# Performance work log

Hardware: AMD Instinct MI355X
Metric: run time of the kernel (lower is better)

The kernel has to match this reference:

```python
import jax, jax.numpy as jnp
import numpy as np

B, QL, KVL, DQ, DKV = 8192, 24, 24, 12, 512


def setup_inputs() -> dict:
    key = jax.random.key(0)
    ks = jax.random.split(key, 9)
    s = lambda fan_in: 1.0 / np.sqrt(fan_in)
    return {
        "q": jax.random.normal(ks[0], (B, QL, DQ), jnp.float32),
        "k": jax.random.normal(ks[1], (B, KVL, DKV), jnp.float32),
        "v": jax.random.normal(ks[2], (B, KVL, DKV), jnp.float32),
        "Wq": jax.random.uniform(ks[3], (DQ, DQ), jnp.float32, -s(DQ), s(DQ)),
        "bq": jax.random.uniform(ks[4], (DQ,), jnp.float32, -s(DQ), s(DQ)),
        "Wk": jax.random.uniform(ks[5], (DQ, DKV), jnp.float32, -s(DKV), s(DKV)),
        "bk": jax.random.uniform(ks[6], (DQ,), jnp.float32, -s(DKV), s(DKV)),
        "Wl": jax.random.uniform(ks[7], (DQ, KVL), jnp.float32, -s(KVL), s(KVL)),
        "bl": jax.random.uniform(ks[8], (DQ,), jnp.float32, -s(KVL), s(KVL)),
    }


def reference(q, k, v, Wq, bq, Wk, bk, Wl, bl):
    # q: [b, q_len, dim_q], k: [b, kv_len, dim_kv]; v is unused (as in source).
    q_proj = jnp.einsum("bqd,ed->bqe", q, Wq) + bq          # [b, q_len, dim_q]
    k_proj = jnp.einsum("bkf,ef->bke", k, Wk) + bk          # [b, kv_len, dim_q]
    qk = jnp.einsum("bqe,bke->bqk", q_proj, k_proj)          # [b, q_len, kv_len]
    a_q = jax.nn.softmax(qk, axis=1)                         # softmax over q_len
    a_k = jax.nn.softmax(qk, axis=2)                         # softmax over kv_len
    c_q = jnp.einsum("bqk,bke->bqe", a_q, k_proj)            # [b, q_len, dim_q]
    qc = jnp.concatenate([q, c_q], axis=2)                   # [b, q_len, 2*dim_q]
    c_k = jnp.einsum("bqk,bqe->bke", a_k, qc)                # [b, kv_len, 2*dim_q]
    # linear over kv_len (== seq_len) dim: c_k^T [b, 2*dim_q, kv_len] -> [b, 2*dim_q, dim_q]
    attn = jnp.einsum("bke,dk->bed", c_k, Wl) + bl
    return attn
```

## Files before the change

### kernel.cpp

```cpp
#include <hip/hip_runtime.h>


typedef short s16x8 __attribute__((ext_vector_type(8)));
typedef float f32x4 __attribute__((ext_vector_type(4)));

__device__ __forceinline__ unsigned perm_hi(float a, float b) {
  return __builtin_amdgcn_perm(__float_as_uint(a), __float_as_uint(b), 0x07060302u);
}

#define DPP_ADD(x, ctrl, rmask)                                                   \
  x += __int_as_float(__builtin_amdgcn_update_dpp(                                \
      0, __float_as_int(x), ctrl, rmask, 0xF, false))

__device__ __forceinline__ float wave_sum64(float x) {
  DPP_ADD(x, 0xB1, 0xF);
  DPP_ADD(x, 0x4E, 0xF);
  DPP_ADD(x, 0x141, 0xF);
  DPP_ADD(x, 0x140, 0xF);
  DPP_ADD(x, 0x142, 0xA);
  DPP_ADD(x, 0x143, 0xC);
  return x;
}

#define DPP_BF(x, OP, ctrl)                                                       \
  {                                                                               \
    float _t = __int_as_float(__builtin_amdgcn_update_dpp(                        \
        0, __float_as_int(x), ctrl, 0xF, 0xF, true));                             \
    x = OP(x, _t);                                                                \
  }
__device__ __forceinline__ float bf32_max(float x) {
  DPP_BF(x, fmaxf, 0xB1);
  DPP_BF(x, fmaxf, 0x4E);
  DPP_BF(x, fmaxf, 0x141);
  DPP_BF(x, fmaxf, 0x140);
  float t = __int_as_float(__builtin_amdgcn_ds_swizzle(__float_as_int(x), 0x401F));
  return fmaxf(x, t);
}
__device__ __forceinline__ float bf32_add(float x) {
  DPP_ADD(x, 0xB1, 0xF);
  DPP_ADD(x, 0x4E, 0xF);
  DPP_ADD(x, 0x141, 0xF);
  DPP_ADD(x, 0x140, 0xF);
  float t = __int_as_float(__builtin_amdgcn_ds_swizzle(__float_as_int(x), 0x401F));
  return x + t;
}

__device__ __forceinline__ float dot12(const float* a, float4 b0, float4 b1, float4 b2) {
  return a[0] * b0.x + a[1] * b0.y + a[2] * b0.z + a[3] * b0.w +
         a[4] * b1.x + a[5] * b1.y + a[6] * b1.z + a[7] * b1.w +
         a[8] * b2.x + a[9] * b2.y + a[10] * b2.z + a[11] * b2.w;
}

__global__ __launch_bounds__(384, 3) void coattn_fused(
    const float* __restrict__ q, const float* __restrict__ k,
    const float* __restrict__ Wq, const float* __restrict__ bq,
    const float* __restrict__ Wk, const float* __restrict__ bk,
    const float* __restrict__ Wl, const float* __restrict__ bl,
    float* __restrict__ out) {
  constexpr int WPAD = 520;

  __shared__ alignas(16) char smemA[12 * WPAD * 2 * 2];
  __shared__ alignas(16) float kpL[96][12];

  short* lwk_hi = (short*)smemA;
  short* lwk_lo = (short*)(smemA + 12 * WPAD * 2);

  const int tid = threadIdx.x;
  const int wave = tid >> 6;
  const int lane = tid & 63;

  for (int i = tid; i < 12 * 512; i += 384) {
    const int e = i >> 9, d = i & 511;
    const float f = Wk[i];
    const unsigned u = __float_as_uint(f);
    const float lo = f - __uint_as_float(u & 0xFFFF0000u);
    lwk_hi[e * WPAD + d] = (short)(u >> 16);
    lwk_lo[e * WPAD + d] = (short)(__float_as_uint(lo) >> 16);
  }
  __syncthreads();

  const int rowL = lane & 15;
  const int kgrp = lane >> 4;
  const int e_eff = (rowL < 12) ? rowL : 11;

  const int r0 = blockIdx.x * 96 + wave * 16;
  const float* abase = k + (size_t)(r0 + rowL) * 512 + kgrp * 8;
  const short* bhi_base = &lwk_hi[e_eff * WPAD + kgrp * 8];
  const short* blo_base = &lwk_lo[e_eff * WPAD + kgrp * 8];

  f32x4 acc = {0.f, 0.f, 0.f, 0.f};

#define COMP(X0, X1, S)                                                            \
  {                                                                                \
    s16x8 bhi = *(const s16x8*)(bhi_base + (S)*32);                                \
    s16x8 blo = *(const s16x8*)(blo_base + (S)*32);                                \
    union { unsigned u[4]; s16x8 v; } ah, al;                                      \
    ah.u[0] = perm_hi((X0).y, (X0).x);                                             \
    ah.u[1] = perm_hi((X0).w, (X0).z);                                             \
    ah.u[2] = perm_hi((X1).y, (X1).x);                                             \
    ah.u[3] = perm_hi((X1).w, (X1).z);                                             \
    float l0 = (X0).x - __uint_as_float(__float_as_uint((X0).x) & 0xFFFF0000u);    \
    float l1 = (X0).y - __uint_as_float(__float_as_uint((X0).y) & 0xFFFF0000u);    \
    float l2 = (X0).z - __uint_as_float(__float_as_uint((X0).z) & 0xFFFF0000u);    \
    float l3 = (X0).w - __uint_as_float(__float_as_uint((X0).w) & 0xFFFF0000u);    \
    float l4 = (X1).x - __uint_as_float(__float_as_uint((X1).x) & 0xFFFF0000u);    \
    float l5 = (X1).y - __uint_as_float(__float_as_uint((X1).y) & 0xFFFF0000u);    \
    float l6 = (X1).z - __uint_as_float(__float_as_uint((X1).z) & 0xFFFF0000u);    \
    float l7 = (X1).w - __uint_as_float(__float_as_uint((X1).w) & 0xFFFF0000u);    \
    al.u[0] = perm_hi(l1, l0);                                                     \
    al.u[1] = perm_hi(l3, l2);                                                     \
    al.u[2] = perm_hi(l5, l4);                                                     \
    al.u[3] = perm_hi(l7, l6);                                                     \
    acc = __builtin_amdgcn_mfma_f32_16x16x32_bf16(ah.v, bhi, acc, 0, 0, 0);        \
    acc = __builtin_amdgcn_mfma_f32_16x16x32_bf16(ah.v, blo, acc, 0, 0, 0);        \
    acc = __builtin_amdgcn_mfma_f32_16x16x32_bf16(al.v, bhi, acc, 0, 0, 0);        \
  }

#define LOADS(SA, SB, R)                                                           \
  SA = *(const float4*)(abase + (R)*32);                                           \
  SB = *(const float4*)(abase + (R)*32 + 4);

  {
    float4 A0a, A0b, A1a, A1b, A2a, A2b, A3a, A3b;
    float4 A4a, A4b, A5a, A5b, A6a, A6b, A7a, A7b;
    LOADS(A0a, A0b, 0)
    LOADS(A1a, A1b, 1)
    LOADS(A2a, A2b, 2)
    LOADS(A3a, A3b, 3)
    LOADS(A4a, A4b, 4)
    LOADS(A5a, A5b, 5)
    LOADS(A6a, A6b, 6)   COMP(A0a, A0b, 0)
    LOADS(A7a, A7b, 7)   COMP(A1a, A1b, 1)
    LOADS(A0a, A0b, 8)   COMP(A2a, A2b, 2)
    LOADS(A1a, A1b, 9)   COMP(A3a, A3b, 3)
    LOADS(A2a, A2b, 10)  COMP(A4a, A4b, 4)
    LOADS(A3a, A3b, 11)  COMP(A5a, A5b, 5)
    LOADS(A4a, A4b, 12)  COMP(A6a, A6b, 6)
    LOADS(A5a, A5b, 13)  COMP(A7a, A7b, 7)
    LOADS(A6a, A6b, 14)  COMP(A0a, A0b, 8)
    LOADS(A7a, A7b, 15)  COMP(A1a, A1b, 9)
    COMP(A2a, A2b, 10)
    COMP(A3a, A3b, 11)
    COMP(A4a, A4b, 12)
    COMP(A5a, A5b, 13)
    COMP(A6a, A6b, 14)
    COMP(A7a, A7b, 15)
  }
#undef LOADS
#undef COMP

  if (rowL < 12) {
    const int lr0 = wave * 16 + kgrp * 4;
#pragma unroll
    for (int i = 0; i < 4; ++i) kpL[lr0 + i][rowL] = acc[i];
  }
  __syncthreads();

  if (wave < 4) {
    float(*qcS)[28] = (float(*)[28])(smemA + (size_t)wave * (24 * 28 * 4));
    float(*GS)[12] = (float(*)[12])(smemA + 4 * (24 * 28 * 4) + (size_t)wave * (24 * 12 * 4));

    const int b = blockIdx.x * 4 + wave;
    const int li = (lane < 24) ? lane : 0;
    const bool act = (lane < 24);
    const int kb0 = wave * 24;

    const float4* WqV = reinterpret_cast<const float4*>(Wq);
    const float4* WlV = reinterpret_cast<const float4*>(Wl);

    float qr[12];
    if (act) {
      const float4* qb = reinterpret_cast<const float4*>(q + (size_t)b * 288 + li * 12);
      float4 t0 = qb[0], t1 = qb[1], t2 = qb[2];
      qr[0] = t0.x; qr[1] = t0.y; qr[2] = t0.z; qr[3] = t0.w;
      qr[4] = t1.x; qr[5] = t1.y; qr[6] = t1.z; qr[7] = t1.w;
      qr[8] = t2.x; qr[9] = t2.y; qr[10] = t2.z; qr[11] = t2.w;
    } else {
#pragma unroll
      for (int d = 0; d < 12; ++d) qr[d] = 0.f;
    }

    float qp_[12];
#pragma unroll
    for (int e = 0; e < 12; ++e) {
      float4 w0 = WqV[e * 3 + 0], w1 = WqV[e * 3 + 1], w2 = WqV[e * 3 + 2];
      qp_[e] = bq[e] + dot12(qr, w0, w1, w2);
    }

    float qbk = 0.f;
#pragma unroll
    for (int e = 0; e < 12; ++e) qbk += qp_[e] * bk[e];

    float qkr[24];
#pragma unroll
    for (int kk = 0; kk < 24; ++kk) {
      float4 k0 = *(const float4*)&kpL[kb0 + kk][0];
      float4 k1 = *(const float4*)&kpL[kb0 + kk][4];
      float4 k2 = *(const float4*)&kpL[kb0 + kk][8];
      qkr[kk] = qbk + dot12(qp_, k0, k1, k2);
    }
    if (lane >= 24) {
#pragma unroll
      for (int j = 0; j < 24; ++j) qkr[j] = -1e30f;
    }

    float akr[24];
    {
      float rm = qkr[0];
#pragma unroll
      for (int j = 1; j < 24; ++j) rm = fmaxf(rm, qkr[j]);
      float s = 0.f;
#pragma unroll
      for (int j = 0; j < 24; ++j) {
        akr[j] = __expf(qkr[j] - rm);
        s += akr[j];
      }
      const float inv = __builtin_amdgcn_rcpf(s);
#pragma unroll
      for (int j = 0; j < 24; ++j) akr[j] *= inv;
    }

    if (lane < 32) {
#pragma unroll
      for (int j = 0; j < 24; ++j) {
        const float m = bf32_max(qkr[j]);
        const float t = __expf(qkr[j] - m);
        const float s2 = bf32_add(t);
        qkr[j] = t * __builtin_amdgcn_rcpf(s2);
      }
    }

    float sa = 0.f;
#pragma unroll
    for (int j = 0; j < 24; ++j) sa += qkr[j];
    float cq[12];
#pragma unroll
    for (int e = 0; e < 12; ++e) cq[e] = bk[e] * sa;
#pragma unroll
    for (int kk = 0; kk < 24; ++kk) {
      float4 k0 = *(const float4*)&kpL[kb0 + kk][0];
      float4 k1 = *(const float4*)&kpL[kb0 + kk][4];
      float4 k2 = *(const float4*)&kpL[kb0 + kk][8];
      const float a = qkr[kk];
      cq[0] += a * k0.x; cq[1] += a * k0.y; cq[2] += a * k0.z; cq[3] += a * k0.w;
      cq[4] += a * k1.x; cq[5] += a * k1.y; cq[6] += a * k1.z; cq[7] += a * k1.w;
      cq[8] += a * k2.x; cq[9] += a * k2.y; cq[10] += a * k2.z; cq[11] += a * k2.w;
    }

    float G[12];
#pragma unroll
    for (int d = 0; d < 12; ++d) {
      float4 w0 = WlV[d * 6 + 0], w1 = WlV[d * 6 + 1], w2 = WlV[d * 6 + 2];
      float4 w3 = WlV[d * 6 + 3], w4 = WlV[d * 6 + 4], w5 = WlV[d * 6 + 5];
      G[d] = akr[0] * w0.x + akr[1] * w0.y + akr[2] * w0.z + akr[3] * w0.w +
             akr[4] * w1.x + akr[5] * w1.y + akr[6] * w1.z + akr[7] * w1.w +
             akr[8] * w2.x + akr[9] * w2.y + akr[10] * w2.z + akr[11] * w2.w +
             akr[12] * w3.x + akr[13] * w3.y + akr[14] * w3.z + akr[15] * w3.w +
             akr[16] * w4.x + akr[17] * w4.y + akr[18] * w4.z + akr[19] * w4.w +
             akr[20] * w5.x + akr[21] * w5.y + akr[22] * w5.z + akr[23] * w5.w;
    }

    if (act) {
      float4 t;
      t.x = qr[0]; t.y = qr[1]; t.z = qr[2]; t.w = qr[3];
      *(float4*)&qcS[li][0] = t;
      t.x = qr[4]; t.y = qr[5]; t.z = qr[6]; t.w = qr[7];
      *(float4*)&qcS[li][4] = t;
      t.x = qr[8]; t.y = qr[9]; t.z = qr[10]; t.w = qr[11];
      *(float4*)&qcS[li][8] = t;
      t.x = cq[0]; t.y = cq[1]; t.z = cq[2]; t.w = cq[3];
      *(float4*)&qcS[li][12] = t;
      t.x = cq[4]; t.y = cq[5]; t.z = cq[6]; t.w = cq[7];
      *(float4*)&qcS[li][16] = t;
      t.x = cq[8]; t.y = cq[9]; t.z = cq[10]; t.w = cq[11];
      *(float4*)&qcS[li][20] = t;
      t.x = G[0]; t.y = G[1]; t.z = G[2]; t.w = G[3];
      *(float4*)&GS[li][0] = t;
      t.x = G[4]; t.y = G[5]; t.z = G[6]; t.w = G[7];
      *(float4*)&GS[li][4] = t;
      t.x = G[8]; t.y = G[9]; t.z = G[10]; t.w = G[11];
      *(float4*)&GS[li][8] = t;
    }

    if (act) {
      float accq[12];
#pragma unroll
      for (int d = 0; d < 12; ++d) accq[d] = bl[d];
#pragma unroll
      for (int q0 = 0; q0 < 24; ++q0) {
        const float qv = qcS[q0][li];
        float4 g0 = *(const float4*)&GS[q0][0];
        float4 g1 = *(const float4*)&GS[q0][4];
        float4 g2 = *(const float4*)&GS[q0][8];
        accq[0] += qv * g0.x; accq[1] += qv * g0.y; accq[2] += qv * g0.z; accq[3] += qv * g0.w;
        accq[4] += qv * g1.x; accq[5] += qv * g1.y; accq[6] += qv * g1.z; accq[7] += qv * g1.w;
        accq[8] += qv * g2.x; accq[9] += qv * g2.y; accq[10] += qv * g2.z; accq[11] += qv * g2.w;
      }
      float* ob = out + (size_t)b * 288 + li * 12;
      float4 w0, w1, w2;
      w0.x = accq[0]; w0.y = accq[1]; w0.z = accq[2]; w0.w = accq[3];
      w1.x = accq[4]; w1.y = accq[5]; w1.z = accq[6]; w1.w = accq[7];
      w2.x = accq[8]; w2.y = accq[9]; w2.z = accq[10]; w2.w = accq[11];
      *(float4*)(ob + 0) = w0;
      *(float4*)(ob + 4) = w1;
      *(float4*)(ob + 8) = w2;
    }
  }
}

__global__ __launch_bounds__(64) void coattn_kernel(
    const float* __restrict__ q, const float* __restrict__ k,
    const float* __restrict__ Wq, const float* __restrict__ bq,
    const float* __restrict__ Wk, const float* __restrict__ bk,
    const float* __restrict__ Wl, const float* __restrict__ bl,
    float* __restrict__ out) {
  constexpr int QL = 24, KVL = 24, DQ = 12, DKV = 512;

  __shared__ alignas(16) float kp[KVL][DQ];
  __shared__ alignas(16) float qc[QL][24];
  __shared__ alignas(16) float akT[KVL][28];
  __shared__ alignas(16) float ckL[KVL][28];
  __shared__ alignas(16) float WqL[DQ][DQ];
  __shared__ alignas(16) float WlT[KVL][DQ];
  __shared__ alignas(16) float bqL[DQ], bkL[DQ], blL[DQ];

  const int lane = threadIdx.x;
  const int b = blockIdx.x;
  const int li = (lane < 24) ? lane : 0;

  for (int p = lane; p < DQ * DQ; p += 64) WqL[p / DQ][p % DQ] = Wq[p];
  for (int p = lane; p < DQ * KVL; p += 64) WlT[p % KVL][p / KVL] = Wl[p];
  const float* qb = q + (size_t)b * (QL * DQ);
  for (int p = lane; p < QL * DQ; p += 64) qc[p / DQ][p % DQ] = qb[p];
  if (lane < DQ) {
    bqL[lane] = bq[lane];
    bkL[lane] = bk[lane];
    blL[lane] = bl[lane];
  }

  const float4* WkV = reinterpret_cast<const float4*>(Wk);
  float4 wk0[DQ], wk1[DQ];
#pragma unroll
  for (int e = 0; e < DQ; ++e) {
    wk0[e] = WkV[e * 128 + lane];
    wk1[e] = WkV[e * 128 + 64 + lane];
  }

  const float4* kbV = reinterpret_cast<const float4*>(k + (size_t)b * (KVL * DKV));

#define KROW(AC, BC, ROW)                                                          \
  {                                                                                \
    float pp[DQ];                                                                  \
    _Pragma("unroll") for (int e = 0; e < DQ; ++e) {                               \
      pp[e] = (AC).x * wk0[e].x + (AC).y * wk0[e].y + (AC).z * wk0[e].z +          \
              (AC).w * wk0[e].w + (BC).x * wk1[e].x + (BC).y * wk1[e].y +          \
              (BC).z * wk1[e].z + (BC).w * wk1[e].w;                               \
    }                                                                              \
    _Pragma("unroll") for (int e = 0; e < DQ; ++e) pp[e] = wave_sum64(pp[e]);      \
    if (lane == 63) {                                                              \
      float4 w0, w1, w2;                                                           \
      w0.x = pp[0]; w0.y = pp[1]; w0.z = pp[2]; w0.w = pp[3];                      \
      w1.x = pp[4]; w1.y = pp[5]; w1.z = pp[6]; w1.w = pp[7];                      \
      w2.x = pp[8]; w2.y = pp[9]; w2.z = pp[10]; w2.w = pp[11];                    \
      *(float4*)&kp[ROW][0] = w0;                                                  \
      *(float4*)&kp[ROW][4] = w1;                                                  \
      *(float4*)&kp[ROW][8] = w2;                                                  \
    }                                                                              \
  }

  float4 A0 = kbV[0 * 128 + lane], B0 = kbV[0 * 128 + 64 + lane];
  float4 A1 = kbV[1 * 128 + lane], B1 = kbV[1 * 128 + 64 + lane];
  float4 A2, B2, A3, B3;
  for (int kv = 0; kv < KVL; kv += 4) {
    {
      const int r = kv + 2;
      A2 = kbV[r * 128 + lane];
      B2 = kbV[r * 128 + 64 + lane];
    }
    KROW(A0, B0, kv);
    {
      const int r = kv + 3;
      A3 = kbV[r * 128 + lane];
      B3 = kbV[r * 128 + 64 + lane];
    }
    KROW(A1, B1, kv + 1);
    {
      const int r = (kv + 4 < KVL) ? kv + 4 : KVL - 1;
      A0 = kbV[r * 128 + lane];
      B0 = kbV[r * 128 + 64 + lane];
    }
    KROW(A2, B2, kv + 2);
    {
      const int r = (kv + 5 < KVL) ? kv + 5 : KVL - 1;
      A1 = kbV[r * 128 + lane];
      B1 = kbV[r * 128 + 64 + lane];
    }
    KROW(A3, B3, kv + 3);
  }
#undef KROW

  float qr[DQ];
  {
    float4 t0 = *(const float4*)&qc[li][0];
    float4 t1 = *(const float4*)&qc[li][4];
    float4 t2 = *(const float4*)&qc[li][8];
    qr[0] = t0.x; qr[1] = t0.y; qr[2] = t0.z; qr[3] = t0.w;
    qr[4] = t1.x; qr[5] = t1.y; qr[6] = t1.z; qr[7] = t1.w;
    qr[8] = t2.x; qr[9] = t2.y; qr[10] = t2.z; qr[11] = t2.w;
  }
  float bqr[DQ];
  {
    float4 t0 = *(const float4*)&bqL[0];
    float4 t1 = *(const float4*)&bqL[4];
    float4 t2 = *(const float4*)&bqL[8];
    bqr[0] = t0.x; bqr[1] = t0.y; bqr[2] = t0.z; bqr[3] = t0.w;
    bqr[4] = t1.x; bqr[5] = t1.y; bqr[6] = t1.z; bqr[7] = t1.w;
    bqr[8] = t2.x; bqr[9] = t2.y; bqr[10] = t2.z; bqr[11] = t2.w;
  }
  float qp_[DQ];
#pragma unroll
  for (int e = 0; e < DQ; ++e) {
    float4 w0 = *(const float4*)&WqL[e][0];
    float4 w1 = *(const float4*)&WqL[e][4];
    float4 w2 = *(const float4*)&WqL[e][8];
    qp_[e] = bqr[e] + dot12(qr, w0, w1, w2);
  }

  float bkr[DQ];
  {
    float4 t0 = *(const float4*)&bkL[0];
    float4 t1 = *(const float4*)&bkL[4];
    float4 t2 = *(const float4*)&bkL[8];
    bkr[0] = t0.x; bkr[1] = t0.y; bkr[2] = t0.z; bkr[3] = t0.w;
    bkr[4] = t1.x; bkr[5] = t1.y; bkr[6] = t1.z; bkr[7] = t1.w;
    bkr[8] = t2.x; bkr[9] = t2.y; bkr[10] = t2.z; bkr[11] = t2.w;
  }
  float qbk = 0.f;
#pragma unroll
  for (int e = 0; e < DQ; ++e) qbk += qp_[e] * bkr[e];

  float qkr[KVL];
#pragma unroll
  for (int kk = 0; kk < KVL; ++kk) {
    float4 k0 = *(const float4*)&kp[kk][0];
    float4 k1 = *(const float4*)&kp[kk][4];
    float4 k2 = *(const float4*)&kp[kk][8];
    qkr[kk] = qbk + dot12(qp_, k0, k1, k2);
  }
  if (lane >= 24 && lane < 32) {
#pragma unroll
    for (int j = 0; j < KVL; ++j) qkr[j] = -1e30f;
  }

  float akr[KVL];
  {
    float rm = qkr[0];
#pragma unroll
    for (int j = 1; j < KVL; ++j) rm = fmaxf(rm, qkr[j]);
    float s = 0.f;
#pragma unroll
    for (int j = 0; j < KVL; ++j) {
      akr[j] = __expf(qkr[j] - rm);
      s += akr[j];
    }
    const float inv = __builtin_amdgcn_rcpf(s);
#pragma unroll
    for (int j = 0; j < KVL; ++j) akr[j] *= inv;
  }

#pragma unroll
  for (int j = 0; j < KVL; ++j) {
    const float m = bf32_max(qkr[j]);
    const float t = __expf(qkr[j] - m);
    const float s2 = bf32_add(t);
    qkr[j] = t * __builtin_amdgcn_rcpf(s2);
  }

  float sa = 0.f;
#pragma unroll
  for (int j = 0; j < KVL; ++j) sa += qkr[j];
  float cq[DQ];
#pragma unroll
  for (int e = 0; e < DQ; ++e) cq[e] = bkr[e] * sa;
#pragma unroll
  for (int kk = 0; kk < KVL; ++kk) {
    float4 k0 = *(const float4*)&kp[kk][0];
    float4 k1 = *(const float4*)&kp[kk][4];
    float4 k2 = *(const float4*)&kp[kk][8];
    const float a = qkr[kk];
    cq[0] += a * k0.x; cq[1] += a * k0.y; cq[2] += a * k0.z; cq[3] += a * k0.w;
    cq[4] += a * k1.x; cq[5] += a * k1.y; cq[6] += a * k1.z; cq[7] += a * k1.w;
    cq[8] += a * k2.x; cq[9] += a * k2.y; cq[10] += a * k2.z; cq[11] += a * k2.w;
  }
  if (lane < 24) {
    float4 w0, w1, w2;
    w0.x = cq[0]; w0.y = cq[1]; w0.z = cq[2]; w0.w = cq[3];
    w1.x = cq[4]; w1.y = cq[5]; w1.z = cq[6]; w1.w = cq[7];
    w2.x = cq[8]; w2.y = cq[9]; w2.z = cq[10]; w2.w = cq[11];
    *(float4*)&qc[li][12] = w0;
    *(float4*)&qc[li][16] = w1;
    *(float4*)&qc[li][20] = w2;
#pragma unroll
    for (int kk = 0; kk < KVL; ++kk) akT[kk][li] = akr[kk];
  }

  float ak[QL];
  {
    float4 a0 = *(const float4*)&akT[li][0];
    float4 a1 = *(const float4*)&akT[li][4];
    float4 a2 = *(const float4*)&akT[li][8];
    float4 a3 = *(const float4*)&akT[li][12];
    float4 a4 = *(const float4*)&akT[li][16];
    float4 a5 = *(const float4*)&akT[li][20];
    ak[0] = a0.x; ak[1] = a0.y; ak[2] = a0.z; ak[3] = a0.w;
    ak[4] = a1.x; ak[5] = a1.y; ak[6] = a1.z; ak[7] = a1.w;
    ak[8] = a2.x; ak[9] = a2.y; ak[10] = a2.z; ak[11] = a2.w;
    ak[12] = a3.x; ak[13] = a3.y; ak[14] = a3.z; ak[15] = a3.w;
    ak[16] = a4.x; ak[17] = a4.y; ak[18] = a4.z; ak[19] = a4.w;
    ak[20] = a5.x; ak[21] = a5.y; ak[22] = a5.z; ak[23] = a5.w;
  }
  float ck[24];
#pragma unroll
  for (int e = 0; e < 24; ++e) ck[e] = 0.f;
#pragma unroll
  for (int qq = 0; qq < QL; ++qq) {
    float4 c0 = *(const float4*)&qc[qq][0];
    float4 c1 = *(const float4*)&qc[qq][4];
    float4 c2 = *(const float4*)&qc[qq][8];
    float4 c3 = *(const float4*)&qc[qq][12];
    float4 c4 = *(const float4*)&qc[qq][16];
    float4 c5 = *(const float4*)&qc[qq][20];
    const float a = ak[qq];
    ck[0] += a * c0.x; ck[1] += a * c0.y; ck[2] += a * c0.z; ck[3] += a * c0.w;
    ck[4] += a * c1.x; ck[5] += a * c1.y; ck[6] += a * c1.z; ck[7] += a * c1.w;
    ck[8] += a * c2.x; ck[9] += a * c2.y; ck[10] += a * c2.z; ck[11] += a * c2.w;
    ck[12] += a * c3.x; ck[13] += a * c3.y; ck[14] += a * c3.z; ck[15] += a * c3.w;
    ck[16] += a * c4.x; ck[17] += a * c4.y; ck[18] += a * c4.z; ck[19] += a * c4.w;
    ck[20] += a * c5.x; ck[21] += a * c5.y; ck[22] += a * c5.z; ck[23] += a * c5.w;
  }
  if (lane < 24) {
    float4 w0, w1, w2, w3, w4, w5;
    w0.x = ck[0]; w0.y = ck[1]; w0.z = ck[2]; w0.w = ck[3];
    w1.x = ck[4]; w1.y = ck[5]; w1.z = ck[6]; w1.w = ck[7];
    w2.x = ck[8]; w2.y = ck[9]; w2.z = ck[10]; w2.w = ck[11];
    w3.x = ck[12]; w3.y = ck[13]; w3.z = ck[14]; w3.w = ck[15];
    w4.x = ck[16]; w4.y = ck[17]; w4.z = ck[18]; w4.w = ck[19];
    w5.x = ck[20]; w5.y = ck[21]; w5.z = ck[22]; w5.w = ck[23];
    *(float4*)&ckL[li][0] = w0;
    *(float4*)&ckL[li][4] = w1;
    *(float4*)&ckL[li][8] = w2;
    *(float4*)&ckL[li][12] = w3;
    *(float4*)&ckL[li][16] = w4;
    *(float4*)&ckL[li][20] = w5;
  }

  float acc[DQ];
  {
    float4 t0 = *(const float4*)&blL[0];
    float4 t1 = *(const float4*)&blL[4];
    float4 t2 = *(const float4*)&blL[8];
    acc[0] = t0.x; acc[1] = t0.y; acc[2] = t0.z; acc[3] = t0.w;
    acc[4] = t1.x; acc[5] = t1.y; acc[6] = t1.z; acc[7] = t1.w;
    acc[8] = t2.x; acc[9] = t2.y; acc[10] = t2.z; acc[11] = t2.w;
  }
#pragma unroll
  for (int kk = 0; kk < KVL; ++kk) {
    const float cv = ckL[kk][li];
    float4 w0 = *(const float4*)&WlT[kk][0];
    float4 w1 = *(const float4*)&WlT[kk][4];
    float4 w2 = *(const float4*)&WlT[kk][8];
    acc[0] += cv * w0.x; acc[1] += cv * w0.y; acc[2] += cv * w0.z; acc[3] += cv * w0.w;
    acc[4] += cv * w1.x; acc[5] += cv * w1.y; acc[6] += cv * w1.z; acc[7] += cv * w1.w;
    acc[8] += cv * w2.x; acc[9] += cv * w2.y; acc[10] += cv * w2.z; acc[11] += cv * w2.w;
  }
  if (lane < 24) {
    float* ob = out + (size_t)b * 288 + li * 12;
    float4 w0, w1, w2;
    w0.x = acc[0]; w0.y = acc[1]; w0.z = acc[2]; w0.w = acc[3];
    w1.x = acc[4]; w1.y = acc[5]; w1.z = acc[6]; w1.w = acc[7];
    w2.x = acc[8]; w2.y = acc[9]; w2.z = acc[10]; w2.w = acc[11];
    *(float4*)(ob + 0) = w0;
    *(float4*)(ob + 4) = w1;
    *(float4*)(ob + 8) = w2;
  }
}

extern "C" void kernel_launch(void* const* d_in, const int* in_sizes, int n_in,
                              void* d_out, int out_size, void* d_ws, size_t ws_size,
                              hipStream_t stream) {
  const float* q = (const float*)d_in[0];
  const float* k = (const float*)d_in[1];
  const float* Wq = (const float*)d_in[3];
  const float* bq = (const float*)d_in[4];
  const float* Wk = (const float*)d_in[5];
  const float* bk = (const float*)d_in[6];
  const float* Wl = (const float*)d_in[7];
  const float* bl = (const float*)d_in[8];
  float* out = (float*)d_out;

  const int B = in_sizes[0] / (24 * 12);

  if ((B % 4) == 0) {
    coattn_fused<<<B / 4, 384, 0, stream>>>(q, k, Wq, bq, Wk, bk, Wl, bl, out);
  } else {
    coattn_kernel<<<B, 64, 0, stream>>>(q, k, Wq, bq, Wk, bk, Wl, bl, out);
  }
}
```

Before: 115.3 us.

## Stage k rows through double-buffered per-wave LDS for coalesced global loads

Global reads of k now follow a row-contiguous pattern: each group of 16 lanes reads 256 contiguous bytes of one row, and the data is written into a per-wave, double-buffered LDS tile. The MFMA operands are then read back from LDS in the layout the bf16 split-precision multiply needs. The aim is better global memory coalescing and load/compute overlap on the bandwidth-bound k projection. In exchange it adds about 52KB of LDS, which likely limits residency to fewer blocks per CU, and it reuses the Wk staging area for kpL.

```diff
diff --git a/kernel.cpp b/kernel.cpp
--- a/kernel.cpp
+++ b/kernel.cpp
@@ -57,13 +57,14 @@
     const float* __restrict__ Wk, const float* __restrict__ bk,
     const float* __restrict__ Wl, const float* __restrict__ bl,
     float* __restrict__ out) {
-  constexpr int WPAD = 520;
-
-  __shared__ alignas(16) char smemA[12 * WPAD * 2 * 2];
-  __shared__ alignas(16) float kpL[96][12];
-
-  short* lwk_hi = (short*)smemA;
-  short* lwk_lo = (short*)(smemA + 12 * WPAD * 2);
+  constexpr int WPADS = 520;
+  constexpr int KSTRF = 68;
+
+  __shared__ alignas(16) char smemW[12 * WPADS * 2 * 2];
+  __shared__ alignas(16) char smemK[6 * 2 * 16 * KSTRF * 4];
+
+  short* lwk_hi = (short*)smemW;
+  short* lwk_lo = (short*)(smemW + 12 * WPADS * 2);
 
   const int tid = threadIdx.x;
   const int wave = tid >> 6;
@@ -74,39 +75,55 @@
     const float f = Wk[i];
     const unsigned u = __float_as_uint(f);
     const float lo = f - __uint_as_float(u & 0xFFFF0000u);
-    lwk_hi[e * WPAD + d] = (short)(u >> 16);
-    lwk_lo[e * WPAD + d] = (short)(__float_as_uint(lo) >> 16);
+    lwk_hi[e * WPADS + d] = (short)(u >> 16);
+    lwk_lo[e * WPADS + d] = (short)(__float_as_uint(lo) >> 16);
   }
   __syncthreads();
 
   const int rowL = lane & 15;
   const int kgrp = lane >> 4;
   const int e_eff = (rowL < 12) ? rowL : 11;
+  const int sub = lane >> 4;
+  const int pos = lane & 15;
 
   const int r0 = blockIdx.x * 96 + wave * 16;
-  const float* abase = k + (size_t)(r0 + rowL) * 512 + kgrp * 8;
-  const short* bhi_base = &lwk_hi[e_eff * WPAD + kgrp * 8];
-  const short* blo_base = &lwk_lo[e_eff * WPAD + kgrp * 8];
+  const float* kg = k + (size_t)(r0 + sub) * 512 + pos * 4;
+  float* kw = (float*)smemK + wave * (2 * 16 * KSTRF);
 
   f32x4 acc = {0.f, 0.f, 0.f, 0.f};
 
-#define COMP(X0, X1, S)                                                            \
+#define LOADU(R, C)                                                                \
+  R##0 = *(const float4*)(kg + 0 * 2048 + (C)*64);                                 \
+  R##1 = *(const float4*)(kg + 1 * 2048 + (C)*64);                                 \
+  R##2 = *(const float4*)(kg + 2 * 2048 + (C)*64);                                 \
+  R##3 = *(const float4*)(kg + 3 * 2048 + (C)*64);
+
+#define WRITEU(R, BUF)                                                             \
+  *(float4*)&kw[(BUF)*16 * KSTRF + (0 * 4 + sub) * KSTRF + pos * 4] = R##0;        \
+  *(float4*)&kw[(BUF)*16 * KSTRF + (1 * 4 + sub) * KSTRF + pos * 4] = R##1;        \
+  *(float4*)&kw[(BUF)*16 * KSTRF + (2 * 4 + sub) * KSTRF + pos * 4] = R##2;        \
+  *(float4*)&kw[(BUF)*16 * KSTRF + (3 * 4 + sub) * KSTRF + pos * 4] = R##3;
+
+#define STEP(C, S)                                                                 \
   {                                                                                \
-    s16x8 bhi = *(const s16x8*)(bhi_base + (S)*32);                                \
-    s16x8 blo = *(const s16x8*)(blo_base + (S)*32);                                \
+    const float* kb = &kw[((C)&1) * 16 * KSTRF];                                   \
+    float4 f0 = *(const float4*)&kb[rowL * KSTRF + kgrp * 8 + (S)*32];             \
+    float4 f1 = *(const float4*)&kb[rowL * KSTRF + kgrp * 8 + (S)*32 + 4];         \
+    s16x8 bhi = *(const s16x8*)(lwk_hi + e_eff * WPADS + kgrp * 8 + (2 * (C) + (S)) * 32); \
+    s16x8 blo = *(const s16x8*)(lwk_lo + e_eff * WPADS + kgrp * 8 + (2 * (C) + (S)) * 32); \
     union { unsigned u[4]; s16x8 v; } ah, al;                                      \
-    ah.u[0] = perm_hi((X0).y, (X0).x);                                             \
-    ah.u[1] = perm_hi((X0).w, (X0).z);                                             \
-    ah.u[2] = perm_hi((X1).y, (X1).x);                                             \
-    ah.u[3] = perm_hi((X1).w, (X1).z);                                             \
-    float l0 = (X0).x - __uint_as_float(__float_as_uint((X0).x) & 0xFFFF0000u);    \
-    float l1 = (X0).y - __uint_as_float(__float_as_uint((X0).y) & 0xFFFF0000u);    \
-    float l2 = (X0).z - __uint_as_float(__float_as_uint((X0).z) & 0xFFFF0000u);    \
-    float l3 = (X0).w - __uint_as_float(__float_as_uint((X0).w) & 0xFFFF0000u);    \
-    float l4 = (X1).x - __uint_as_float(__float_as_uint((X1).x) & 0xFFFF0000u);    \
-    float l5 = (X1).y - __uint_as_float(__float_as_uint((X1).y) & 0xFFFF0000u);    \
-    float l6 = (X1).z - __uint_as_float(__float_as_uint((X1).z) & 0xFFFF0000u);    \
-    float l7 = (X1).w - __uint_as_float(__float_as_uint((X1).w) & 0xFFFF0000u);    \
+    ah.u[0] = perm_hi(f0.y, f0.x);                                                 \
+    ah.u[1] = perm_hi(f0.w, f0.z);                                                 \
+    ah.u[2] = perm_hi(f1.y, f1.x);                                                 \
+    ah.u[3] = perm_hi(f1.w, f1.z);                                                 \
+    float l0 = f0.x - __uint_as_float(__float_as_uint(f0.x) & 0xFFFF0000u);        \
+    float l1 = f0.y - __uint_as_float(__float_as_uint(f0.y) & 0xFFFF0000u);        \
+    float l2 = f0.z - __uint_as_float(__float_as_uint(f0.z) & 0xFFFF0000u);        \
+    float l3 = f0.w - __uint_as_float(__float_as_uint(f0.w) & 0xFFFF0000u);        \
+    float l4 = f1.x - __uint_as_float(__float_as_uint(f1.x) & 0xFFFF0000u);        \
+    float l5 = f1.y - __uint_as_float(__float_as_uint(f1.y) & 0xFFFF0000u);        \
+    float l6 = f1.z - __uint_as_float(__float_as_uint(f1.z) & 0xFFFF0000u);        \
+    float l7 = f1.w - __uint_as_float(__float_as_uint(f1.w) & 0xFFFF0000u);        \
     al.u[0] = perm_hi(l1, l0);                                                     \
     al.u[1] = perm_hi(l3, l2);                                                     \
     al.u[2] = perm_hi(l5, l4);                                                     \
@@ -116,39 +133,29 @@
     acc = __builtin_amdgcn_mfma_f32_16x16x32_bf16(al.v, bhi, acc, 0, 0, 0);        \
   }
 
-#define LOADS(SA, SB, R)                                                           \
-  SA = *(const float4*)(abase + (R)*32);                                           \
-  SB = *(const float4*)(abase + (R)*32 + 4);
+#define COMPUTE(C) STEP(C, 0) STEP(C, 1)
 
   {
-    float4 A0a, A0b, A1a, A1b, A2a, A2b, A3a, A3b;
-    float4 A4a, A4b, A5a, A5b, A6a, A6b, A7a, A7b;
-    LOADS(A0a, A0b, 0)
-    LOADS(A1a, A1b, 1)
-    LOADS(A2a, A2b, 2)
-    LOADS(A3a, A3b, 3)
-    LOADS(A4a, A4b, 4)
-    LOADS(A5a, A5b, 5)
-    LOADS(A6a, A6b, 6)   COMP(A0a, A0b, 0)
-    LOADS(A7a, A7b, 7)   COMP(A1a, A1b, 1)
-    LOADS(A0a, A0b, 8)   COMP(A2a, A2b, 2)
-    LOADS(A1a, A1b, 9)   COMP(A3a, A3b, 3)
-    LOADS(A2a, A2b, 10)  COMP(A4a, A4b, 4)
-    LOADS(A3a, A3b, 11)  COMP(A5a, A5b, 5)
-    LOADS(A4a, A4b, 12)  COMP(A6a, A6b, 6)
-    LOADS(A5a, A5b, 13)  COMP(A7a, A7b, 7)
-    LOADS(A6a, A6b, 14)  COMP(A0a, A0b, 8)
-    LOADS(A7a, A7b, 15)  COMP(A1a, A1b, 9)
-    COMP(A2a, A2b, 10)
-    COMP(A3a, A3b, 11)
-    COMP(A4a, A4b, 12)
-    COMP(A5a, A5b, 13)
-    COMP(A6a, A6b, 14)
-    COMP(A7a, A7b, 15)
-  }
-#undef LOADS
-#undef COMP
-
+    float4 X0, X1, X2, X3, Y0, Y1, Y2, Y3;
+    LOADU(X, 0)
+    LOADU(Y, 1)
+    WRITEU(X, 0)
+    LOADU(X, 2)  WRITEU(Y, 1)  COMPUTE(0)
+    LOADU(Y, 3)  WRITEU(X, 0)  COMPUTE(1)
+    LOADU(X, 4)  WRITEU(Y, 1)  COMPUTE(2)
+    LOADU(Y, 5)  WRITEU(X, 0)  COMPUTE(3)
+    LOADU(X, 6)  WRITEU(Y, 1)  COMPUTE(4)
+    LOADU(Y, 7)  WRITEU(X, 0)  COMPUTE(5)
+    WRITEU(Y, 1)  COMPUTE(6)
+    COMPUTE(7)
+  }
+#undef LOADU
+#undef WRITEU
+#undef STEP
+#undef COMPUTE
+
+  __syncthreads();
+  float(*kpL)[12] = (float(*)[12])smemW;
   if (rowL < 12) {
     const int lr0 = wave * 16 + kgrp * 4;
 #pragma unroll
@@ -157,8 +164,8 @@
   __syncthreads();
 
   if (wave < 4) {
-    float(*qcS)[28] = (float(*)[28])(smemA + (size_t)wave * (24 * 28 * 4));
-    float(*GS)[12] = (float(*)[12])(smemA + 4 * (24 * 28 * 4) + (size_t)wave * (24 * 12 * 4));
+    float(*qcS)[28] = (float(*)[28])(smemK + (size_t)wave * (24 * 28 * 4));
+    float(*GS)[12] = (float(*)[12])(smemK + 4 * (24 * 28 * 4) + (size_t)wave * (24 * 12 * 4));
 
     const int b = blockIdx.x * 4 + wave;
     const int li = (lane < 24) ? lane : 0;
```

Measured after the change: 116.9 us. About the same (+1.4%).
